# Kernel tuning notes

Hardware: AMD Instinct MI355X
Metric: run time of the kernel (lower is better)

Reference implementation:

```python
import jax, jax.numpy as jnp
import numpy as np
import math

EMBED_DIM = 1024
N1 = 8192
N2 = 8192

def setup_inputs() -> dict:
    key = jax.random.key(0)
    ks = jax.random.split(key, 16)
    D = EMBED_DIM
    s = 1.0 / math.sqrt(D)
    inp = {
        "input_tensor1": jax.random.normal(ks[0], (N1, D), jnp.float32),
        "input_tensor2": jax.random.normal(ks[1], (N2, D), jnp.float32),
    }
    names = ["q1", "k1", "v1", "q2", "k2", "v2"]
    for i, n in enumerate(names):
        inp[f"W{n}"] = jax.random.normal(ks[2 + 2 * i], (D, D), jnp.float32) * s
        inp[f"b{n}"] = jax.random.normal(ks[3 + 2 * i], (D,), jnp.float32) * 0.01
    return inp

def reference(input_tensor1, input_tensor2,
              Wq1, bq1, Wk1, bk1, Wv1, bv1,
              Wq2, bq2, Wk2, bk2, Wv2, bv2):
    D = Wq1.shape[0]
    scale = 1.0 / math.sqrt(D)
    # projections (torch Linear: x @ W^T + b; here W stored pre-transposed)
    q1 = input_tensor1 @ Wq1 + bq1   # [N1, D]
    k1 = input_tensor1 @ Wk1 + bk1   # [N1, D]
    v1 = input_tensor1 @ Wv1 + bv1   # [N1, D]
    q2 = input_tensor2 @ Wq2 + bq2   # [N2, D]
    k2 = input_tensor2 @ Wk2 + bk2   # [N2, D]
    v2 = input_tensor2 @ Wv2 + bv2   # [N2, D]
    # direction 1: tensor2 queries attend to tensor1 keys/values
    probs1 = jax.nn.sigmoid((q2 @ k1.T) * scale)   # [N2, N1]
    ctx1 = probs1 @ v1                              # [N2, D]
    # direction 2: tensor1 queries attend to tensor2 keys/values
    probs2 = jax.nn.sigmoid((q1 @ k2.T) * scale)   # [N1, N2]
    ctx2 = probs2 @ v2                              # [N1, D]
    return (ctx2, probs2, ctx1, probs1)
```

## Files before the change

kernel.cpp:

```cpp
#include <hip/hip_runtime.h>
#include <hip/hip_bf16.h>

#define DIM   1024
#define NTOK  8192

using bf16 = __hip_bfloat16;
typedef __attribute__((ext_vector_type(8))) short bf16x8;
typedef __attribute__((ext_vector_type(4))) float f32x4;

__device__ __forceinline__ unsigned short f2b(float x) {
  union { __hip_bfloat16 h; unsigned short u; } cv;
  cv.h = __float2bfloat16(x);
  return cv.u;
}

__global__ __launch_bounds__(256) void cast_f32_bf16(const float* __restrict__ in,
                                                     bf16* __restrict__ out, int n4) {
  int i = blockIdx.x * 256 + threadIdx.x;
  if (i < n4) {
    const float4 v = ((const float4*)in)[i];
    ushort4 p;
    p.x = f2b(v.x); p.y = f2b(v.y); p.z = f2b(v.z); p.w = f2b(v.w);
    ((ushort4*)out)[i] = p;
  }
}

__global__ __launch_bounds__(256) void transpose_cast32(const float* __restrict__ in,
                                                        bf16* __restrict__ out, int R, int C) {
  __shared__ float t[32][33];
  const int tilesC = C / 32;
  const int c0 = (blockIdx.x % tilesC) * 32;
  const int r0 = (blockIdx.x / tilesC) * 32;
  const int tx = threadIdx.x & 31, ty = threadIdx.x >> 5;
  #pragma unroll
  for (int i = 0; i < 4; ++i) {
    int r = ty + i * 8;
    t[r][tx] = in[(size_t)(r0 + r) * C + c0 + tx];
  }
  __syncthreads();
  #pragma unroll
  for (int i = 0; i < 4; ++i) {
    int cr = ty + i * 8;
    out[(size_t)(c0 + cr) * R + r0 + tx] = __float2bfloat16(t[tx][cr]);
  }
}

__global__ __launch_bounds__(256) void pack_bias(const float* b0, const float* b1,
                                                 const float* b2, const float* b3,
                                                 const float* b4, const float* b5,
                                                 float* __restrict__ out) {
  int i = blockIdx.x * 256 + threadIdx.x;
  if (i < 6 * DIM) {
    int s = i >> 10, o = i & 1023;
    const float* p = (s == 0) ? b0 : (s == 1) ? b1 : (s == 2) ? b2 : (s == 3) ? b3 : (s == 4) ? b4 : b5;
    out[i] = p[o];
  }
}

__global__ __launch_bounds__(256) void add2_f32(const float* __restrict__ a,
                                                const float* __restrict__ b,
                                                float* __restrict__ o, int n4) {
  int i = blockIdx.x * 256 + threadIdx.x;
  if (i < n4) {
    float4 x = ((const float4*)a)[i];
    float4 y = ((const float4*)b)[i];
    x.x += y.x; x.y += y.y; x.z += y.z; x.w += y.w;
    ((float4*)o)[i] = x;
  }
}

template<int EPI>
__global__ __launch_bounds__(512, 2) void gemm256(
    const bf16* __restrict__ A, const bf16* __restrict__ Bt, const bf16* __restrict__ Bt2,
    int M, int N, int K, int tilesN, int ks,
    const float* __restrict__ bias, const float* __restrict__ bias2, float scale,
    float* __restrict__ Cf, bf16* __restrict__ Cb,
    bf16* __restrict__ Cq, bf16* __restrict__ Ck, bf16* __restrict__ Cv,
    bf16* __restrict__ Cq2, bf16* __restrict__ Ck2, bf16* __restrict__ Cv2)
{
  __shared__ bf16 lds[2][2 * 16384];
  const int t    = threadIdx.x;
  const int lane = t & 63, wid = t >> 6;
  const int wr = wid >> 2, wc = wid & 3;
  const int lr = lane & 15, kg = lane >> 4;

  const int nwg = gridDim.x;
  int bid = blockIdx.x;
  { const int q = nwg >> 3; bid = (bid & 7) * q + (bid >> 3); }
  const int per = nwg / ks;
  const int z   = bid / per;
  const int rem = bid % per;
  const int bm  = (rem / tilesN) << 8;
  const int bn  = (rem % tilesN) << 8;
  const int Kc  = K / ks;
  const int NT  = Kc >> 6;
  const size_t kb = (size_t)z * Kc;

  const bf16* BtU = Bt;
  const float* biasU = bias;
  bf16 *CqU = Cq, *CkU = Ck, *CvU = Cv;
  int bmL = bm;
  if (EPI == 5 && bm >= (M >> 1)) {
    BtU = Bt2; biasU = bias2; CqU = Cq2; CkU = Ck2; CvU = Cv2; bmL = bm - (M >> 1);
  }

  const int srow = t >> 3;
  const int scol = ((t & 7) ^ (srow & 7)) * 8;
  const size_t bA = (size_t)(bm + srow) * K + kb + scol;
  const size_t bB = (size_t)(bn + srow) * K + kb + scol;

#define STAGE(buf, isB, R0, tt_) do {                                                   \
    const bf16* g_ = ((isB) ? BtU + bB : A + bA) + (size_t)(R0) * K + (size_t)(tt_) * 64; \
    __builtin_amdgcn_global_load_lds(                                                   \
        (const __attribute__((address_space(1))) unsigned int*)g_,                      \
        (__attribute__((address_space(3))) unsigned int*)(&lds[buf][((isB) ? 16384 : 0) + (R0) * 64 + t * 8]), \
        16, 0, 0);                                                                      \
  } while (0)

  const int fcol0 = ((kg)     ^ (lr & 7)) * 8;
  const int fcol1 = ((4 + kg) ^ (lr & 7)) * 8;
  const int arow = (wr * 128 + lr) * 64;
  const int brow = (wc * 64 + lr) * 64;

  f32x4 acc[8][4] = {};

  STAGE(0, false, 0, 0);   STAGE(0, false, 128, 0);
  STAGE(0, false, 64, 0);  STAGE(0, false, 192, 0);
  STAGE(0, true, 0, 0);    STAGE(0, true, 64, 0);
  STAGE(0, true, 128, 0);  STAGE(0, true, 192, 0);
  if (NT > 1) {
    STAGE(1, false, 0, 1); STAGE(1, false, 128, 1);
    STAGE(1, true, 0, 1);  STAGE(1, true, 64, 1);
    asm volatile("s_waitcnt vmcnt(4)" ::: "memory");
  } else {
    asm volatile("s_waitcnt vmcnt(0)" ::: "memory");
  }
  __builtin_amdgcn_sched_barrier(0);
  __builtin_amdgcn_s_barrier();

  for (int tt = 0; tt < NT; ++tt) {
    const int cur = tt & 1;
    const bf16* bufA = &lds[cur][0];
    const bf16* bufB = &lds[cur][16384];
    bf16x8 b0[4], b1[4];

    {
      bf16x8 a[4];
      #pragma unroll
      for (int n = 0; n < 4; ++n) b0[n] = *(const bf16x8*)(bufB + brow + n * 1024 + fcol0);
      #pragma unroll
      for (int mi = 0; mi < 4; ++mi) a[mi] = *(const bf16x8*)(bufA + arow + mi * 1024 + fcol0);
      if (tt + 1 < NT) { STAGE(cur ^ 1, true, 128, tt + 1); STAGE(cur ^ 1, true, 192, tt + 1); }
      __builtin_amdgcn_s_barrier();
      asm volatile("s_waitcnt lgkmcnt(0)" ::: "memory");
      __builtin_amdgcn_sched_barrier(0);
      __builtin_amdgcn_s_setprio(1);
      #pragma unroll
      for (int mi = 0; mi < 4; ++mi)
        #pragma unroll
        for (int n = 0; n < 4; ++n)
          acc[mi][n] = __builtin_amdgcn_mfma_f32_16x16x32_bf16(a[mi], b0[n], acc[mi][n], 0, 0, 0);
      __builtin_amdgcn_s_setprio(0);
      __builtin_amdgcn_s_barrier();
    }
    {
      bf16x8 a[4];
      #pragma unroll
      for (int n = 0; n < 4; ++n) b1[n] = *(const bf16x8*)(bufB + brow + n * 1024 + fcol1);
      #pragma unroll
      for (int mi = 0; mi < 4; ++mi) a[mi] = *(const bf16x8*)(bufA + arow + mi * 1024 + fcol1);
      if (tt + 1 < NT) { STAGE(cur ^ 1, false, 64, tt + 1); STAGE(cur ^ 1, false, 192, tt + 1); }
      __builtin_amdgcn_s_barrier();
      asm volatile("s_waitcnt lgkmcnt(0)" ::: "memory");
      __builtin_amdgcn_sched_barrier(0);
      __builtin_amdgcn_s_setprio(1);
      #pragma unroll
      for (int mi = 0; mi < 4; ++mi)
        #pragma unroll
        for (int n = 0; n < 4; ++n)
          acc[mi][n] = __builtin_amdgcn_mfma_f32_16x16x32_bf16(a[mi], b1[n], acc[mi][n], 0, 0, 0);
      __builtin_amdgcn_s_setprio(0);
      __builtin_amdgcn_s_barrier();
    }
    {
      bf16x8 a[4];
      #pragma unroll
      for (int mi = 0; mi < 4; ++mi) a[mi] = *(const bf16x8*)(bufA + arow + 4096 + mi * 1024 + fcol0);
      if (tt + 2 < NT) { STAGE(cur, false, 0, tt + 2); STAGE(cur, false, 128, tt + 2); }
      __builtin_amdgcn_s_barrier();
      asm volatile("s_waitcnt lgkmcnt(0)" ::: "memory");
      __builtin_amdgcn_sched_barrier(0);
      __builtin_amdgcn_s_setprio(1);
      #pragma unroll
      for (int mi = 0; mi < 4; ++mi)
        #pragma unroll
        for (int n = 0; n < 4; ++n)
          acc[4 + mi][n] = __builtin_amdgcn_mfma_f32_16x16x32_bf16(a[mi], b0[n], acc[4 + mi][n], 0, 0, 0);
      __builtin_amdgcn_s_setprio(0);
      __builtin_amdgcn_s_barrier();
    }
    {
      bf16x8 a[4];
      #pragma unroll
      for (int mi = 0; mi < 4; ++mi) a[mi] = *(const bf16x8*)(bufA + arow + 4096 + mi * 1024 + fcol1);
      if (tt + 2 < NT) { STAGE(cur, true, 0, tt + 2); STAGE(cur, true, 64, tt + 2); }
      __builtin_amdgcn_s_barrier();
      asm volatile("s_waitcnt lgkmcnt(0)" ::: "memory");
      __builtin_amdgcn_sched_barrier(0);
      __builtin_amdgcn_s_setprio(1);
      #pragma unroll
      for (int mi = 0; mi < 4; ++mi)
        #pragma unroll
        for (int n = 0; n < 4; ++n)
          acc[4 + mi][n] = __builtin_amdgcn_mfma_f32_16x16x32_bf16(a[mi], b1[n], acc[4 + mi][n], 0, 0, 0);
      __builtin_amdgcn_s_setprio(0);
      if (tt + 2 < NT) { asm volatile("s_waitcnt vmcnt(4)" ::: "memory"); }
      else             { asm volatile("s_waitcnt vmcnt(0)" ::: "memory"); }
      __builtin_amdgcn_sched_barrier(0);
      __builtin_amdgcn_s_barrier();
    }
  }
#undef STAGE

  const int er = wr * 128 + kg * 4;
  const int ec = bn + wc * 64 + lr;

  if (EPI == 2 || EPI == 4) {
    #pragma unroll
    for (int m = 0; m < 8; ++m) {
      #pragma unroll
      for (int n = 0; n < 4; ++n) {
        const int c = ec + n * 16;
        #pragma unroll
        for (int e = 0; e < 4; ++e) {
          const size_t idx = (size_t)(bm + er + m * 16 + e) * N + c;
          float pr = 1.0f / (1.0f + __expf(-acc[m][n][e] * scale));
          Cf[idx] = pr;
          if (EPI == 4) Cb[idx] = __float2bfloat16(pr);
        }
      }
    }
  } else if (EPI == 3) {
    float* Cz = Cf + (size_t)z * ((size_t)M * N);
    #pragma unroll
    for (int m = 0; m < 8; ++m)
      #pragma unroll
      for (int n = 0; n < 4; ++n)
        #pragma unroll
        for (int e = 0; e < 4; ++e)
          Cz[(size_t)(bm + er + m * 16 + e) * N + ec + n * 16] = acc[m][n][e];
  } else if (EPI == 5) {
    const int seg = bn >> 10;
    #pragma unroll
    for (int m = 0; m < 8; ++m) {
      #pragma unroll
      for (int n = 0; n < 4; ++n) {
        const int c  = ec + n * 16;
        const int cl = c & 1023;
        const float b = biasU[c];
        #pragma unroll
        for (int e = 0; e < 4; ++e) {
          const int r = bmL + er + m * 16 + e;
          const float val = acc[m][n][e] + b;
          if (seg == 0)      CqU[(size_t)r * DIM + cl] = __float2bfloat16(val);
          else if (seg == 1) CkU[(size_t)r * DIM + cl] = __float2bfloat16(val);
          else               CvU[(size_t)cl * NTOK + r] = __float2bfloat16(val);
        }
      }
    }
  }
}

template<int EPI, bool A_F32>
__global__ __launch_bounds__(256) void gemm_nt(
    const void* __restrict__ Ap, const bf16* __restrict__ Bt,
    int M, int N, int K,
    const float* __restrict__ bias, float scale,
    float* __restrict__ Cf, bf16* __restrict__ Cb)
{
  __shared__ bf16 As[128 * 32];
  __shared__ bf16 Bs[128 * 32];
  const int tid  = threadIdx.x;
  const int lane = tid & 63, wid = tid >> 6;
  const int wr = wid >> 1, wc = wid & 1;
  const int tilesN = N >> 7;
  const int nwg = gridDim.x;
  int bid = blockIdx.x;
  if ((nwg & 7) == 0) { const int q = nwg >> 3; bid = (bid & 7) * q + (bid >> 3); }
  const int bm = (bid / tilesN) * 128, bn = (bid % tilesN) * 128;
  f32x4 acc[4][4] = {};
  const bf16*  Ab16 = (const bf16*)Ap;
  const float* Af32 = (const float*)Ap;
  const int srow = tid >> 2, sc8 = (tid & 3) * 8;
  const int frow = tid >> 3, fc4 = (tid & 7) * 4;

  for (int k0 = 0; k0 < K; k0 += 32) {
    if (A_F32) {
      #pragma unroll
      for (int is = 0; is < 4; ++is) {
        int row = is * 32 + frow;
        const float4 v = *(const float4*)(Af32 + (size_t)(bm + row) * K + k0 + fc4);
        ushort4 p; p.x = f2b(v.x); p.y = f2b(v.y); p.z = f2b(v.z); p.w = f2b(v.w);
        *(ushort4*)(&As[row * 32 + fc4]) = p;
      }
    } else {
      #pragma unroll
      for (int is = 0; is < 2; ++is) {
        int row = is * 64 + srow;
        const bf16* g = Ab16 + (size_t)(bm + row) * K + k0 + sc8;
        __builtin_amdgcn_global_load_lds(
            (const __attribute__((address_space(1))) unsigned int*)g,
            (__attribute__((address_space(3))) unsigned int*)(&As[row * 32 + sc8]), 16, 0, 0);
      }
    }
    #pragma unroll
    for (int is = 0; is < 2; ++is) {
      int row = is * 64 + srow;
      const bf16* g = Bt + (size_t)(bn + row) * K + k0 + sc8;
      __builtin_amdgcn_global_load_lds(
          (const __attribute__((address_space(1))) unsigned int*)g,
          (__attribute__((address_space(3))) unsigned int*)(&Bs[row * 32 + sc8]), 16, 0, 0);
    }
    __syncthreads();
    const int lr = lane & 15, kg = lane >> 4;
    bf16x8 af[4], bfv[4];
    #pragma unroll
    for (int i = 0; i < 4; ++i)
      af[i] = *(const bf16x8*)(&As[(wr * 64 + i * 16 + lr) * 32 + kg * 8]);
    #pragma unroll
    for (int j = 0; j < 4; ++j)
      bfv[j] = *(const bf16x8*)(&Bs[(wc * 64 + j * 16 + lr) * 32 + kg * 8]);
    #pragma unroll
    for (int i = 0; i < 4; ++i)
      #pragma unroll
      for (int j = 0; j < 4; ++j)
        acc[i][j] = __builtin_amdgcn_mfma_f32_16x16x32_bf16(af[i], bfv[j], acc[i][j], 0, 0, 0);
    __syncthreads();
  }
  const int r0 = bm + wr * 64 + (lane >> 4) * 4;
  const int c0 = bn + wc * 64 + (lane & 15);
  if (EPI == 2) {
    #pragma unroll
    for (int i = 0; i < 4; ++i)
      #pragma unroll
      for (int j = 0; j < 4; ++j)
        #pragma unroll
        for (int e = 0; e < 4; ++e) {
          float pr = 1.0f / (1.0f + __expf(-acc[i][j][e] * scale));
          Cf[(size_t)(r0 + i * 16 + e) * N + c0 + j * 16] = pr;
        }
  } else {
    #pragma unroll
    for (int i = 0; i < 4; ++i)
      #pragma unroll
      for (int j = 0; j < 4; ++j)
        #pragma unroll
        for (int e = 0; e < 4; ++e)
          Cf[(size_t)(r0 + i * 16 + e) * N + c0 + j * 16] = acc[i][j][e];
  }
}

extern "C" void kernel_launch(void* const* d_in, const int* in_sizes, int n_in,
                              void* d_out, int out_size, void* d_ws, size_t ws_size,
                              hipStream_t stream) {
  const float* x1 = (const float*)d_in[0];
  const float* x2 = (const float*)d_in[1];
  const float* W[6] = { (const float*)d_in[2],  (const float*)d_in[4],  (const float*)d_in[6],
                        (const float*)d_in[8],  (const float*)d_in[10], (const float*)d_in[12] };
  const float* B[6] = { (const float*)d_in[3],  (const float*)d_in[5],  (const float*)d_in[7],
                        (const float*)d_in[9],  (const float*)d_in[11], (const float*)d_in[13] };

  const size_t MD = (size_t)NTOK * DIM;
  const size_t DD = (size_t)DIM * DIM;
  const size_t NN = (size_t)NTOK * NTOK;

  bf16* ws   = (bf16*)d_ws;
  bf16* x1b  = ws;
  bf16* x2b  = x1b + MD;
  bf16* wt1  = x2b + MD;
  bf16* wt2  = wt1 + 3 * DD;
  float* bstack = (float*)(wt2 + 3 * DD);
  bf16* q1   = wt2 + 3 * DD + 16384;
  bf16* k1   = q1 + MD;
  bf16* v1T  = k1 + MD;
  bf16* q2   = v1T + MD;
  bf16* k2   = q2 + MD;
  bf16* v2T  = k2 + MD;
  bf16* probsb = v2T + MD;
  float* part  = (float*)(probsb + NN);

  const size_t baseB  = (size_t)((8 * MD) + 6 * DD + 16384) * 2;
  const size_t tierBB = baseB + NN * 2;
  const size_t tierAB = tierBB + 2 * MD * 4;
  const bool hasProbsB = (ws_size >= tierBB);
  const bool hasSplitK = (ws_size >= tierAB);

  float* out    = (float*)d_out;
  float* ctx2   = out;
  float* probs2 = ctx2 + MD;
  float* ctx1   = probs2 + NN;
  float* probs1 = ctx1 + MD;

  const float scale = 1.0f / 32.0f;

  {
    int n4 = (int)(MD / 4);
    int blks = (n4 + 255) / 256;
    cast_f32_bf16<<<blks, 256, 0, stream>>>(x1, x1b, n4);
    cast_f32_bf16<<<blks, 256, 0, stream>>>(x2, x2b, n4);
  }
  {
    int blks = (DIM / 32) * (DIM / 32);
    transpose_cast32<<<blks, 256, 0, stream>>>(W[0], wt1 + 0 * DD, DIM, DIM);
    transpose_cast32<<<blks, 256, 0, stream>>>(W[1], wt1 + 1 * DD, DIM, DIM);
    transpose_cast32<<<blks, 256, 0, stream>>>(W[2], wt1 + 2 * DD, DIM, DIM);
    transpose_cast32<<<blks, 256, 0, stream>>>(W[3], wt2 + 0 * DD, DIM, DIM);
    transpose_cast32<<<blks, 256, 0, stream>>>(W[4], wt2 + 1 * DD, DIM, DIM);
    transpose_cast32<<<blks, 256, 0, stream>>>(W[5], wt2 + 2 * DD, DIM, DIM);
  }
  pack_bias<<<24, 256, 0, stream>>>(B[0], B[1], B[2], B[3], B[4], B[5], bstack);

  gemm256<5><<<64 * 12, 512, 0, stream>>>(
      x1b, wt1, wt2, 2 * NTOK, 3 * DIM, DIM, 12, 1,
      bstack, bstack + 3 * DIM, 0.f,
      nullptr, nullptr, q1, k1, v1T, q2, k2, v2T);

  const int gQK = (NTOK / 256) * (NTOK / 256);
  const int gPV1 = (NTOK / 256) * (DIM / 256);

  if (hasProbsB) {
    gemm256<4><<<gQK, 512, 0, stream>>>(q1, k2, nullptr, NTOK, NTOK, DIM, 32, 1,
        nullptr, nullptr, scale, probs2, probsb,
        nullptr, nullptr, nullptr, nullptr, nullptr, nullptr);
    if (hasSplitK) {
      gemm256<3><<<2 * gPV1, 512, 0, stream>>>(probsb, v2T, nullptr, NTOK, DIM, NTOK, 4, 2,
          nullptr, nullptr, 0.f, part, nullptr,
          nullptr, nullptr, nullptr, nullptr, nullptr, nullptr);
      add2_f32<<<(int)(MD / 4 + 255) / 256, 256, 0, stream>>>(part, part + MD, ctx2, (int)(MD / 4));
    } else {
      gemm256<3><<<gPV1, 512, 0, stream>>>(probsb, v2T, nullptr, NTOK, DIM, NTOK, 4, 1,
          nullptr, nullptr, 0.f, ctx2, nullptr,
          nullptr, nullptr, nullptr, nullptr, nullptr, nullptr);
    }
    gemm256<4><<<gQK, 512, 0, stream>>>(q2, k1, nullptr, NTOK, NTOK, DIM, 32, 1,
        nullptr, nullptr, scale, probs1, probsb,
        nullptr, nullptr, nullptr, nullptr, nullptr, nullptr);
    if (hasSplitK) {
      gemm256<3><<<2 * gPV1, 512, 0, stream>>>(probsb, v1T, nullptr, NTOK, DIM, NTOK, 4, 2,
          nullptr, nullptr, 0.f, part, nullptr,
          nullptr, nullptr, nullptr, nullptr, nullptr, nullptr);
      add2_f32<<<(int)(MD / 4 + 255) / 256, 256, 0, stream>>>(part, part + MD, ctx1, (int)(MD / 4));
    } else {
      gemm256<3><<<gPV1, 512, 0, stream>>>(probsb, v1T, nullptr, NTOK, DIM, NTOK, 4, 1,
          nullptr, nullptr, 0.f, ctx1, nullptr,
          nullptr, nullptr, nullptr, nullptr, nullptr, nullptr);
    }
  } else {
    const int gs = (NTOK / 128) * (NTOK / 128);
    const int gp = (NTOK / 128) * (DIM / 128);
    gemm_nt<2, false><<<gs, 256, 0, stream>>>(q1, k2, NTOK, NTOK, DIM, nullptr, scale, probs2, nullptr);
    gemm_nt<3, true ><<<gp, 256, 0, stream>>>(probs2, v2T, NTOK, DIM, NTOK, nullptr, 0.f, ctx2, nullptr);
    gemm_nt<2, false><<<gs, 256, 0, stream>>>(q2, k1, NTOK, NTOK, DIM, nullptr, scale, probs1, nullptr);
    gemm_nt<3, true ><<<gp, 256, 0, stream>>>(probs1, v1T, NTOK, DIM, NTOK, nullptr, 0.f, ctx1, nullptr);
  }
}
```

Measured before the change: 855.9 us.

## Stage GEMM epilogues through LDS, merge both attention directions into single launches

Each GEMM epilogue now writes the accumulator tile into LDS and then stores coalesced 16-byte rows to global memory, replacing scattered scalar stores. The projection GEMM writes V row-major and a new bf16 LDS transpose kernel produces V^T, avoiding strided transposed stores. Both QK^T sigmoid GEMMs run as one dual-direction launch with separate bf16 probability buffers, and the two split-K partial reductions are merged into one add kernel. This costs more workspace and an extra transpose pass, and the fallback path changes when workspace is insufficient.

Measured after the change: 831.6 us. -2.8%, faster.

```diff
diff --git a/kernel.cpp b/kernel.cpp
--- a/kernel.cpp
+++ b/kernel.cpp
@@ -45,6 +45,39 @@
   }
 }
 
+__global__ __launch_bounds__(256) void transpose_bf16(const short* __restrict__ in,
+                                                      short* __restrict__ out,
+                                                      const short* __restrict__ in2,
+                                                      short* __restrict__ out2,
+                                                      int R, int C) {
+  __shared__ short t[64][72];
+  const int tilesC = C >> 6;
+  const int tilesPer = (R >> 6) * tilesC;
+  int bid = blockIdx.x;
+  const short* src = in; short* dst = out;
+  if (bid >= tilesPer) { bid -= tilesPer; src = in2; dst = out2; }
+  const int r0 = (bid / tilesC) << 6, c0 = (bid % tilesC) << 6;
+  const int tr = threadIdx.x >> 3, tc8 = (threadIdx.x & 7) << 3;
+  #pragma unroll
+  for (int p = 0; p < 2; ++p) {
+    int r = tr + p * 32;
+    int sc = tc8 ^ (((r >> 3) & 7) << 3);
+    *(bf16x8*)&t[r][sc] = *(const bf16x8*)&src[(size_t)(r0 + r) * C + c0 + tc8];
+  }
+  __syncthreads();
+  #pragma unroll
+  for (int p = 0; p < 2; ++p) {
+    int oc = tr + p * 32;
+    bf16x8 v;
+    #pragma unroll
+    for (int e = 0; e < 8; ++e) {
+      int a = tc8 + e;
+      v[e] = t[a][oc ^ (((a >> 3) & 7) << 3)];
+    }
+    *(bf16x8*)&dst[(size_t)(c0 + oc) * R + r0 + tc8] = v;
+  }
+}
+
 __global__ __launch_bounds__(256) void pack_bias(const float* b0, const float* b1,
                                                  const float* b2, const float* b3,
                                                  const float* b4, const float* b5,
@@ -57,24 +90,29 @@
   }
 }
 
-__global__ __launch_bounds__(256) void add2_f32(const float* __restrict__ a,
-                                                const float* __restrict__ b,
-                                                float* __restrict__ o, int n4) {
+__global__ __launch_bounds__(256) void add2_dual(const float* __restrict__ p,
+                                                 float* __restrict__ o0,
+                                                 float* __restrict__ o1, int n4) {
+  const size_t MD = (size_t)NTOK * DIM;
   int i = blockIdx.x * 256 + threadIdx.x;
-  if (i < n4) {
-    float4 x = ((const float4*)a)[i];
-    float4 y = ((const float4*)b)[i];
-    x.x += y.x; x.y += y.y; x.z += y.z; x.w += y.w;
-    ((float4*)o)[i] = x;
-  }
-}
-
-template<int EPI>
+  if (i < 2 * n4) {
+    int d = i >= n4;
+    int j = i - d * n4;
+    const float4 a = ((const float4*)(p + (size_t)d * 2 * MD))[j];
+    const float4 b = ((const float4*)(p + (size_t)d * 2 * MD + MD))[j];
+    float4 r; r.x = a.x + b.x; r.y = a.y + b.y; r.z = a.z + b.z; r.w = a.w + b.w;
+    ((float4*)(d ? o1 : o0))[j] = r;
+  }
+}
+
+template<int EPI, bool DUAL>
 __global__ __launch_bounds__(512, 2) void gemm256(
-    const bf16* __restrict__ A, const bf16* __restrict__ Bt, const bf16* __restrict__ Bt2,
-    int M, int N, int K, int tilesN, int ks,
+    const bf16* __restrict__ A,  const bf16* __restrict__ Bt,
+    const bf16* __restrict__ A2, const bf16* __restrict__ Bt2,
+    int M, int N, int K, int tilesN, int ks, int perDir,
     const float* __restrict__ bias, const float* __restrict__ bias2, float scale,
-    float* __restrict__ Cf, bf16* __restrict__ Cb,
+    float* __restrict__ Cf, float* __restrict__ Cf2,
+    bf16* __restrict__ Cb, bf16* __restrict__ Cb2,
     bf16* __restrict__ Cq, bf16* __restrict__ Ck, bf16* __restrict__ Cv,
     bf16* __restrict__ Cq2, bf16* __restrict__ Ck2, bf16* __restrict__ Cv2)
 {
@@ -87,16 +125,20 @@
   const int nwg = gridDim.x;
   int bid = blockIdx.x;
   { const int q = nwg >> 3; bid = (bid & 7) * q + (bid >> 3); }
-  const int per = nwg / ks;
-  const int z   = bid / per;
-  const int rem = bid % per;
+
+  const bf16* Au = A; const bf16* BtU = Bt;
+  float* CfU = Cf; bf16* CbU = Cb;
+  int bidL = bid;
+  if (DUAL && bidL >= perDir) { bidL -= perDir; Au = A2; BtU = Bt2; CfU = Cf2; CbU = Cb2; }
+  const int per = perDir / ks;
+  const int z   = bidL / per;
+  const int rem = bidL % per;
   const int bm  = (rem / tilesN) << 8;
   const int bn  = (rem % tilesN) << 8;
   const int Kc  = K / ks;
   const int NT  = Kc >> 6;
   const size_t kb = (size_t)z * Kc;
 
-  const bf16* BtU = Bt;
   const float* biasU = bias;
   bf16 *CqU = Cq, *CkU = Ck, *CvU = Cv;
   int bmL = bm;
@@ -110,7 +152,7 @@
   const size_t bB = (size_t)(bn + srow) * K + kb + scol;
 
 #define STAGE(buf, isB, R0, tt_) do {                                                   \
-    const bf16* g_ = ((isB) ? BtU + bB : A + bA) + (size_t)(R0) * K + (size_t)(tt_) * 64; \
+    const bf16* g_ = ((isB) ? BtU + bB : Au + bA) + (size_t)(R0) * K + (size_t)(tt_) * 64; \
     __builtin_amdgcn_global_load_lds(                                                   \
         (const __attribute__((address_space(1))) unsigned int*)g_,                      \
         (__attribute__((address_space(3))) unsigned int*)(&lds[buf][((isB) ? 16384 : 0) + (R0) * 64 + t * 8]), \
@@ -222,52 +264,64 @@
   }
 #undef STAGE
 
-  const int er = wr * 128 + kg * 4;
-  const int ec = bn + wc * 64 + lr;
-
-  if (EPI == 2 || EPI == 4) {
-    #pragma unroll
-    for (int m = 0; m < 8; ++m) {
-      #pragma unroll
-      for (int n = 0; n < 4; ++n) {
-        const int c = ec + n * 16;
-        #pragma unroll
-        for (int e = 0; e < 4; ++e) {
-          const size_t idx = (size_t)(bm + er + m * 16 + e) * N + c;
-          float pr = 1.0f / (1.0f + __expf(-acc[m][n][e] * scale));
-          Cf[idx] = pr;
-          if (EPI == 4) Cb[idx] = __float2bfloat16(pr);
+  float* Lf = (float*)&lds[0][0];
+
+  float bN[4];
+  if (EPI == 5) {
+    #pragma unroll
+    for (int n = 0; n < 4; ++n) bN[n] = biasU[bn + wc * 64 + n * 16 + lr];
+  }
+
+  #pragma unroll
+  for (int h = 0; h < 2; ++h) {
+    if (wr == h) {
+      #pragma unroll
+      for (int m = 0; m < 8; ++m)
+        #pragma unroll
+        for (int n = 0; n < 4; ++n)
+          #pragma unroll
+          for (int e = 0; e < 4; ++e) {
+            const int lrow = kg * 4 + m * 16 + e;
+            const int lcol = wc * 64 + n * 16 + lr;
+            float v = acc[m][n][e];
+            if (EPI == 2 || EPI == 4) v = 1.0f / (1.0f + __expf(-v * scale));
+            if (EPI == 5) v += bN[n];
+            Lf[lrow * 256 + (lcol ^ (((lrow >> 2) & 3) << 4))] = v;
+          }
+    }
+    __syncthreads();
+    #pragma unroll
+    for (int rr = 0; rr < 2; ++rr) {
+      const int lrow = wid * 16 + rr * 8 + (lane >> 3);
+      (void)lrow;
+    }
+    #pragma unroll
+    for (int rr = 0; rr < 16; ++rr) {
+      const int lrow = wid * 16 + rr;
+      const int cb   = lane * 4;
+      const int cbs  = cb ^ (((lrow >> 2) & 3) << 4);
+      const f32x4 v  = *(const f32x4*)&Lf[lrow * 256 + cbs];
+      const int gr   = bm + h * 128 + lrow;
+      const int gc   = bn + cb;
+      if (EPI == 2 || EPI == 4) {
+        *(f32x4*)&CfU[(size_t)gr * N + gc] = v;
+        if (EPI == 4) {
+          ushort4 p; p.x = f2b(v[0]); p.y = f2b(v[1]); p.z = f2b(v[2]); p.w = f2b(v[3]);
+          *(ushort4*)&CbU[(size_t)gr * N + gc] = p;
         }
+      } else if (EPI == 3) {
+        float* Cz = CfU + (size_t)z * ((size_t)M * N);
+        *(f32x4*)&Cz[(size_t)gr * N + gc] = v;
+      } else if (EPI == 5) {
+        const int seg = bn >> 10;
+        const int cl  = (bn & 1023) + cb;
+        const int r   = bmL + h * 128 + lrow;
+        bf16* sel = (seg == 0) ? CqU : (seg == 1) ? CkU : CvU;
+        ushort4 p; p.x = f2b(v[0]); p.y = f2b(v[1]); p.z = f2b(v[2]); p.w = f2b(v[3]);
+        *(ushort4*)&sel[(size_t)r * DIM + cl] = p;
       }
     }
-  } else if (EPI == 3) {
-    float* Cz = Cf + (size_t)z * ((size_t)M * N);
-    #pragma unroll
-    for (int m = 0; m < 8; ++m)
-      #pragma unroll
-      for (int n = 0; n < 4; ++n)
-        #pragma unroll
-        for (int e = 0; e < 4; ++e)
-          Cz[(size_t)(bm + er + m * 16 + e) * N + ec + n * 16] = acc[m][n][e];
-  } else if (EPI == 5) {
-    const int seg = bn >> 10;
-    #pragma unroll
-    for (int m = 0; m < 8; ++m) {
-      #pragma unroll
-      for (int n = 0; n < 4; ++n) {
-        const int c  = ec + n * 16;
-        const int cl = c & 1023;
-        const float b = biasU[c];
-        #pragma unroll
-        for (int e = 0; e < 4; ++e) {
-          const int r = bmL + er + m * 16 + e;
-          const float val = acc[m][n][e] + b;
-          if (seg == 0)      CqU[(size_t)r * DIM + cl] = __float2bfloat16(val);
-          else if (seg == 1) CkU[(size_t)r * DIM + cl] = __float2bfloat16(val);
-          else               CvU[(size_t)cl * NTOK + r] = __float2bfloat16(val);
-        }
-      }
-    }
+    __syncthreads();
   }
 }
 
@@ -275,8 +329,7 @@
 __global__ __launch_bounds__(256) void gemm_nt(
     const void* __restrict__ Ap, const bf16* __restrict__ Bt,
     int M, int N, int K,
-    const float* __restrict__ bias, float scale,
-    float* __restrict__ Cf, bf16* __restrict__ Cb)
+    float scale, float* __restrict__ Cf)
 {
   __shared__ bf16 As[128 * 32];
   __shared__ bf16 Bs[128 * 32];
@@ -382,18 +435,17 @@
   float* bstack = (float*)(wt2 + 3 * DD);
   bf16* q1   = wt2 + 3 * DD + 16384;
   bf16* k1   = q1 + MD;
-  bf16* v1T  = k1 + MD;
-  bf16* q2   = v1T + MD;
+  bf16* q2   = k1 + MD;
   bf16* k2   = q2 + MD;
-  bf16* v2T  = k2 + MD;
+  bf16* v1r  = k2 + MD;
+  bf16* v2r  = v1r + MD;
+  bf16* v1T  = v2r + MD;
+  bf16* v2T  = v1T + MD;
   bf16* probsb = v2T + MD;
-  float* part  = (float*)(probsb + NN);
-
-  const size_t baseB  = (size_t)((8 * MD) + 6 * DD + 16384) * 2;
-  const size_t tierBB = baseB + NN * 2;
-  const size_t tierAB = tierBB + 2 * MD * 4;
-  const bool hasProbsB = (ws_size >= tierBB);
-  const bool hasSplitK = (ws_size >= tierAB);
+  float* part  = (float*)(probsb + 2 * NN);
+
+  const size_t topBytes = ((size_t)(12 * MD + 6 * DD + 16384) + 2 * NN) * 2 + 4 * MD * 4;
+  const bool top = (ws_size >= topBytes);
 
   float* out    = (float*)d_out;
   float* ctx2   = out;
@@ -420,47 +472,52 @@
   }
   pack_bias<<<24, 256, 0, stream>>>(B[0], B[1], B[2], B[3], B[4], B[5], bstack);
 
-  gemm256<5><<<64 * 12, 512, 0, stream>>>(
-      x1b, wt1, wt2, 2 * NTOK, 3 * DIM, DIM, 12, 1,
+  gemm256<5, false><<<64 * 12, 512, 0, stream>>>(
+      x1b, wt1, nullptr, wt2, 2 * NTOK, 3 * DIM, DIM, 12, 1, 768,
       bstack, bstack + 3 * DIM, 0.f,
-      nullptr, nullptr, q1, k1, v1T, q2, k2, v2T);
-
-  const int gQK = (NTOK / 256) * (NTOK / 256);
-  const int gPV1 = (NTOK / 256) * (DIM / 256);
-
-  if (hasProbsB) {
-    gemm256<4><<<gQK, 512, 0, stream>>>(q1, k2, nullptr, NTOK, NTOK, DIM, 32, 1,
-        nullptr, nullptr, scale, probs2, probsb,
+      nullptr, nullptr, nullptr, nullptr,
+      q1, k1, v1r, q2, k2, v2r);
+
+  transpose_bf16<<<2 * (NTOK / 64) * (DIM / 64), 256, 0, stream>>>(
+      (const short*)v1r, (short*)v1T, (const short*)v2r, (short*)v2T, NTOK, DIM);
+
+  const int perQK = (NTOK / 256) * (NTOK / 256);
+  const int perPV = (NTOK / 256) * (DIM / 256);
+
+  if (top) {
+    gemm256<4, true><<<2 * perQK, 512, 0, stream>>>(
+        q1, k2, q2, k1, NTOK, NTOK, DIM, 32, 1, perQK,
+        nullptr, nullptr, scale,
+        probs2, probs1, probsb, probsb + NN,
         nullptr, nullptr, nullptr, nullptr, nullptr, nullptr);
-    if (hasSplitK) {
-      gemm256<3><<<2 * gPV1, 512, 0, stream>>>(probsb, v2T, nullptr, NTOK, DIM, NTOK, 4, 2,
-          nullptr, nullptr, 0.f, part, nullptr,
-          nullptr, nullptr, nullptr, nullptr, nullptr, nullptr);
-      add2_f32<<<(int)(MD / 4 + 255) / 256, 256, 0, stream>>>(part, part + MD, ctx2, (int)(MD / 4));
-    } else {
-      gemm256<3><<<gPV1, 512, 0, stream>>>(probsb, v2T, nullptr, NTOK, DIM, NTOK, 4, 1,
-          nullptr, nullptr, 0.f, ctx2, nullptr,
-          nullptr, nullptr, nullptr, nullptr, nullptr, nullptr);
-    }
-    gemm256<4><<<gQK, 512, 0, stream>>>(q2, k1, nullptr, NTOK, NTOK, DIM, 32, 1,
-        nullptr, nullptr, scale, probs1, probsb,
+    gemm256<3, false><<<2 * perPV, 512, 0, stream>>>(
+        probsb, v2T, nullptr, nullptr, NTOK, DIM, NTOK, 4, 2, 2 * perPV,
+        nullptr, nullptr, 0.f,
+        part, nullptr, nullptr, nullptr,
         nullptr, nullptr, nullptr, nullptr, nullptr, nullptr);
-    if (hasSplitK) {
-      gemm256<3><<<2 * gPV1, 512, 0, stream>>>(probsb, v1T, nullptr, NTOK, DIM, NTOK, 4, 2,
-          nullptr, nullptr, 0.f, part, nullptr,
-          nullptr, nullptr, nullptr, nullptr, nullptr, nullptr);
-      add2_f32<<<(int)(MD / 4 + 255) / 256, 256, 0, stream>>>(part, part + MD, ctx1, (int)(MD / 4));
-    } else {
-      gemm256<3><<<gPV1, 512, 0, stream>>>(probsb, v1T, nullptr, NTOK, DIM, NTOK, 4, 1,
-          nullptr, nullptr, 0.f, ctx1, nullptr,
-          nullptr, nullptr, nullptr, nullptr, nullptr, nullptr);
+    gemm256<3, false><<<2 * perPV, 512, 0, stream>>>(
+        probsb + NN, v1T, nullptr, nullptr, NTOK, DIM, NTOK, 4, 2, 2 * perPV,
+        nullptr, nullptr, 0.f,
+        part + 2 * MD, nullptr, nullptr, nullptr,
+        nullptr, nullptr, nullptr, nullptr, nullptr, nullptr);
+    {
+      int n4 = (int)(MD / 4);
+      add2_dual<<<(2 * n4 + 255) / 256, 256, 0, stream>>>(part, ctx2, ctx1, n4);
     }
   } else {
-    const int gs = (NTOK / 128) * (NTOK / 128);
-    const int gp = (NTOK / 128) * (DIM / 128);
-    gemm_nt<2, false><<<gs, 256, 0, stream>>>(q1, k2, NTOK, NTOK, DIM, nullptr, scale, probs2, nullptr);
-    gemm_nt<3, true ><<<gp, 256, 0, stream>>>(probs2, v2T, NTOK, DIM, NTOK, nullptr, 0.f, ctx2, nullptr);
-    gemm_nt<2, false><<<gs, 256, 0, stream>>>(q2, k1, NTOK, NTOK, DIM, nullptr, scale, probs1, nullptr);
-    gemm_nt<3, true ><<<gp, 256, 0, stream>>>(probs1, v1T, NTOK, DIM, NTOK, nullptr, 0.f, ctx1, nullptr);
-  }
-}
+    gemm256<2, false><<<perQK, 512, 0, stream>>>(
+        q1, k2, nullptr, nullptr, NTOK, NTOK, DIM, 32, 1, perQK,
+        nullptr, nullptr, scale,
+        probs2, nullptr, nullptr, nullptr,
+        nullptr, nullptr, nullptr, nullptr, nullptr, nullptr);
+    gemm_nt<3, true><<<(NTOK / 128) * (DIM / 128), 256, 0, stream>>>(
+        probs2, v2T, NTOK, DIM, NTOK, 0.f, ctx2);
+    gemm256<2, false><<<perQK, 512, 0, stream>>>(
+        q2, k1, nullptr, nullptr, NTOK, NTOK, DIM, 32, 1, perQK,
+        nullptr, nullptr, scale,
+        probs1, nullptr, nullptr, nullptr,
+        nullptr, nullptr, nullptr, nullptr, nullptr, nullptr);
+    gemm_nt<3, true><<<(NTOK / 128) * (DIM / 128), 256, 0, stream>>>(
+        probs1, v1T, NTOK, DIM, NTOK, 0.f, ctx1);
+  }
+}
```
